# Performance work log

Measured on AMD Instinct MI355X. Metric: run time of the kernel, lower is better.

Reference implementation:

```python
import jax, jax.numpy as jnp
import numpy as np

B, N, IN, LAT, HID = 64, 128, 5, 3, 64
ALPHA = 0.1
NEG_SLOPE = 0.2  # GATv2Conv default negative_slope


def _w(key, fan_in, shape):
    return jax.random.normal(key, shape, jnp.float32) * (1.0 / np.sqrt(fan_in))


def setup_inputs():
    key = jax.random.key(0)
    ks = iter(jax.random.split(key, 64))
    d = {}
    d["batch"] = jax.random.normal(next(ks), (B, N, IN), jnp.float32)
    d["enc_w1"] = _w(next(ks), IN, (IN, HID));   d["enc_b1"] = jnp.zeros((HID,), jnp.float32)
    d["enc_w2"] = _w(next(ks), HID, (HID, HID)); d["enc_b2"] = jnp.zeros((HID,), jnp.float32)
    d["enc_w3"] = _w(next(ks), HID, (HID, LAT)); d["enc_b3"] = jnp.zeros((LAT,), jnp.float32)
    for i, cin in zip((1, 2, 3, 4), (1, HID, HID, HID)):
        d[f"g{i}_wl"] = _w(next(ks), cin, (cin, HID)); d[f"g{i}_bl"] = jnp.zeros((HID,), jnp.float32)
        d[f"g{i}_wr"] = _w(next(ks), cin, (cin, HID)); d[f"g{i}_br"] = jnp.zeros((HID,), jnp.float32)
        d[f"g{i}_att"] = _w(next(ks), HID, (HID,));    d[f"g{i}_b"] = jnp.zeros((HID,), jnp.float32)
    d["lab_w"] = _w(next(ks), HID, (HID, 4)); d["lab_b"] = jnp.zeros((4,), jnp.float32)
    d["val_w"] = _w(next(ks), HID, (HID, 1)); d["val_b"] = jnp.zeros((1,), jnp.float32)
    d["skip_w"] = _w(next(ks), LAT, (LAT, HID)); d["skip_b"] = jnp.zeros((HID,), jnp.float32)
    return d


def _gabriel_adj(p):
    """Gabriel graph adjacency, p: [N, LAT] -> bool [N, N] (symmetric, no diag).
    Edge (i,j) survives iff no witness k with |p_k - mid_ij|^2 < |p_i - p_j|^2 / 4."""
    n = p.shape[0]
    mid = 0.5 * (p[:, None, :] + p[None, :, :])                      # [n,n,d]
    r2 = 0.25 * jnp.sum((p[:, None, :] - p[None, :, :]) ** 2, -1)    # [n,n]
    pk2 = jnp.sum(p * p, -1)                                         # [n]
    m2 = jnp.sum(mid * mid, -1)                                      # [n,n]
    # d2[k,i,j] = |p_k - mid_ij|^2 via expansion (avoids [n,n,n,d] tensor)
    d2 = pk2[:, None, None] - 2.0 * jnp.einsum('kd,ijd->kij', p, mid) + m2[None]
    idx = jnp.arange(n)
    not_ij = (idx[:, None, None] != idx[None, :, None]) & (idx[:, None, None] != idx[None, None, :])
    blocked = jnp.any((d2 < r2[None]) & not_ij, axis=0)              # [n,n]
    return (~blocked) & (idx[:, None] != idx[None, :])


def _gatv2(x, adj, wl, bl, wr, br, att, b):
    """Dense single-head GATv2 (PyG GATv2Conv semantics, self-loops already in adj).
    x: [B,N,Cin], adj: bool [B,N,N] (adj[b,i,j] => edge j->i)."""
    hl = x @ wl + bl   # source transform (lin_l)
    hr = x @ wr + br   # target transform (lin_r)
    e = jax.nn.leaky_relu(hr[:, :, None, :] + hl[:, None, :, :], NEG_SLOPE)  # [B,i,j,H]
    s = jnp.einsum('bijh,h->bij', e, att)
    s = jnp.where(adj, s, -1e30)
    a = jax.nn.softmax(s, axis=-1)                                   # softmax over neighbors j of i
    return jnp.einsum('bij,bjh->bih', a, hl) + b


def reference(batch, enc_w1, enc_b1, enc_w2, enc_b2, enc_w3, enc_b3,
              g1_wl, g1_bl, g1_wr, g1_br, g1_att, g1_b,
              g2_wl, g2_bl, g2_wr, g2_br, g2_att, g2_b,
              g3_wl, g3_bl, g3_wr, g3_br, g3_att, g3_b,
              g4_wl, g4_bl, g4_wr, g4_br, g4_att, g4_b,
              lab_w, lab_b, val_w, val_b, skip_w, skip_b):
    relu = jax.nn.relu
    h = relu(batch @ enc_w1 + enc_b1)
    h = relu(h @ enc_w2 + enc_b2)
    latent = h @ enc_w3 + enc_b3                                     # [B,N,3]

    adj = jax.vmap(_gabriel_adj)(jax.lax.stop_gradient(latent))      # bool [B,N,N]
    adj_sl = adj | jnp.eye(N, dtype=bool)                            # add_self_loops=True

    x0 = latent[..., 2:3]                                            # node feature = 3rd latent coord
    x1 = relu(_gatv2(x0, adj_sl, g1_wl, g1_bl, g1_wr, g1_br, g1_att, g1_b))
    x2 = relu(_gatv2(x1, adj_sl, g2_wl, g2_bl, g2_wr, g2_br, g2_att, g2_b))
    skip = latent @ skip_w + skip_b
    x3 = relu(_gatv2(x2, adj_sl, g3_wl, g3_bl, g3_wr, g3_br, g3_att, g3_b) + ALPHA * skip)
    logits = x3 @ lab_w + lab_b                                      # [B,N,4]
    x4 = relu(_gatv2(x2, adj_sl, g4_wl, g4_bl, g4_wr, g4_br, g4_att, g4_b) + ALPHA * skip)
    values = x4 @ val_w + val_b                                      # [B,N,1]

    # dense edge attributes: pairwise latent distances masked by the Gabriel adjacency
    d2p = jnp.sum((latent[:, :, None, :] - latent[:, None, :, :]) ** 2, -1)
    edge_dist = jnp.sqrt(jnp.where(adj, d2p, 1.0)) * adj

    return (batch[:, :, :4], batch[:, :, 4:5], logits, values, latent, adj, edge_dist)
```

## Files before the change

### kernel.cpp

```cpp
#include <hip/hip_runtime.h>

#define BB 64
#define NN 128
#define INF_ 5
#define LATD 3
#define HIDD 64

__global__ __launch_bounds__(256) void enc_kernel(
    const float* __restrict__ batch,
    const float* __restrict__ w1, const float* __restrict__ b1,
    const float* __restrict__ w2, const float* __restrict__ b2,
    const float* __restrict__ w3, const float* __restrict__ b3,
    double* __restrict__ aos,
    float* __restrict__ o0, float* __restrict__ o1, float* __restrict__ o4)
{
    const int b = blockIdx.x;
    const int n0 = blockIdx.y * 32;
    const int tid = threadIdx.x;
    const int w = tid >> 6, lane = tid & 63;

    __shared__ double xs[32][6];
    __shared__ double w1s[INF_][HIDD];
    __shared__ float  w2s[HIDD * HIDD];
    __shared__ double w3s[HIDD][LATD];
    __shared__ double b1s[HIDD], b2s[HIDD], b3s[LATD];

    for (int idx = tid; idx < 32 * INF_; idx += 256) {
        int n = idx / INF_, c = idx % INF_;
        float v = batch[((size_t)b * NN + n0 + n) * INF_ + c];
        xs[n][c] = (double)v;
        if (c < 4) o0[((size_t)b * NN + n0 + n) * 4 + c] = v;
        else       o1[(size_t)b * NN + n0 + n] = v;
    }
    for (int idx = tid; idx < INF_ * HIDD; idx += 256)
        w1s[idx / HIDD][idx % HIDD] = (double)w1[idx];
    for (int idx = tid; idx < HIDD * HIDD; idx += 256)
        w2s[idx] = w2[idx];
    for (int idx = tid; idx < HIDD * LATD; idx += 256)
        w3s[idx / LATD][idx % LATD] = (double)w3[idx];
    if (tid < HIDD) {
        b1s[tid] = (double)b1[tid];
        b2s[tid] = (double)b2[tid];
    }
    if (tid < LATD) b3s[tid] = (double)b3[tid];
    __syncthreads();

    for (int r = 0; r < 8; ++r) {
        const int nl = w * 8 + r;
        const int n = n0 + nl;
        double h1v = b1s[lane];
        for (int k = 0; k < INF_; ++k) h1v += xs[nl][k] * w1s[k][lane];
        h1v = fmax(h1v, 0.0);
        double h2v = b2s[lane];
        for (int k = 0; k < HIDD; ++k) {
            double h1k = __shfl(h1v, k, 64);
            h2v += h1k * (double)w2s[k * HIDD + lane];
        }
        h2v = fmax(h2v, 0.0);
        double l0 = h2v * w3s[lane][0];
        double l1 = h2v * w3s[lane][1];
        double l2 = h2v * w3s[lane][2];
        for (int o = 32; o >= 1; o >>= 1) {
            l0 += __shfl_xor(l0, o, 64);
            l1 += __shfl_xor(l1, o, 64);
            l2 += __shfl_xor(l2, o, 64);
        }
        l0 += b3s[0]; l1 += b3s[1]; l2 += b3s[2];
        if (lane == 0) {
            double* A = aos + ((size_t)b * NN + n) * 4;
            A[0] = l0; A[1] = l1; A[2] = l2;
            A[3] = l0 * l0 + l1 * l1 + l2 * l2;
        }
        if (lane < LATD) {
            double lv = (lane == 0) ? l0 : ((lane == 1) ? l1 : l2);
            o4[((size_t)b * NN + n) * LATD + lane] = (float)lv;
        }
    }
}

__global__ __launch_bounds__(256) void gabriel_kernel(
    const double* __restrict__ aos,
    float* __restrict__ o5, float* __restrict__ o6)
{
    const int b = blockIdx.y;
    const int w = threadIdx.x >> 6, lane = threadIdx.x & 63;
    const int v = blockIdx.x * 4 + w;

    __shared__ double4 Ps[NN];
    const double2* src = (const double2*)(aos + (size_t)b * NN * 4);
    double2* dst = (double2*)Ps;
    for (int idx = threadIdx.x; idx < NN * 2; idx += 256) dst[idx] = src[idx];
    __syncthreads();

    const double4 A  = Ps[lane];
    const double4 Bq = Ps[lane + 64];

    for (int half = 0; half < 2; ++half) {
        const int i = (half == 0) ? v : 126 - v;
        if (half == 1 && i == v) break;
        const int jstart = (half == 0) ? (v + 1) : (127 - v);
        const double4 pi = Ps[i];
        const double aix = A.x - pi.x,  aiy = A.y - pi.y,  aiz = A.z - pi.z;
        const double bix = Bq.x - pi.x, biy = Bq.y - pi.y, biz = Bq.z - pi.z;
        const bool mA = (lane != i), mB = (lane + 64 != i);
        for (int j = jstart; j < NN; ++j) {
            double4 pj = Ps[j];
            double ajx = A.x - pj.x,  ajy = A.y - pj.y,  ajz = A.z - pj.z;
            double bjx = Bq.x - pj.x, bjy = Bq.y - pj.y, bjz = Bq.z - pj.z;
            double dA = aix * ajx + aiy * ajy + aiz * ajz;
            double dB = bix * bjx + biy * bjy + biz * bjz;
            bool tA = (dA < 0.0) && mA && (lane != j);
            bool tB = (dB < 0.0) && mB && (lane + 64 != j);
            if (!__any(tA || tB)) {
                if (lane == 0) {
                    double dx = pi.x - pj.x, dy = pi.y - pj.y, dz = pi.z - pj.z;
                    float d = (float)sqrt(dx * dx + dy * dy + dz * dz);
                    size_t ij = ((size_t)b * NN + i) * NN + j;
                    size_t ji = ((size_t)b * NN + j) * NN + i;
                    o5[ij] = 1.0f; o5[ji] = 1.0f;
                    o6[ij] = d;    o6[ji] = d;
                }
            }
        }
    }
}

template <int CIN>
__global__ __launch_bounds__(256) void lin_kernel(
    const float* __restrict__ xin,
    const float* __restrict__ latf,
    const float* __restrict__ wl, const float* __restrict__ bl,
    const float* __restrict__ wr, const float* __restrict__ br,
    float* __restrict__ hl, float* __restrict__ hr)
{
    const int bx = blockIdx.x;
    const int b = bx >> 2, n0 = (bx & 3) << 5;
    const int tid = threadIdx.x, w = tid >> 6, lane = tid & 63;
    __shared__ float4 xs4[(CIN == 64) ? 32 * 16 : 8];
    float* xsh = (float*)xs4;

    if constexpr (CIN == 64) {
        const float4* src = (const float4*)(xin + ((size_t)b * NN + n0) * HIDD);
        for (int idx = tid; idx < 32 * 16; idx += 256) xs4[idx] = src[idx];
    } else {
        if (tid < 32) xsh[tid] = latf[((size_t)b * NN + n0 + tid) * LATD + 2];
    }
    __syncthreads();

    float wc[CIN];
    #pragma unroll
    for (int k = 0; k < CIN; ++k) wc[k] = wl[k * HIDD + lane];
    float bv = bl[lane];
    for (int m = 0; m < 8; ++m) {
        int nl = w * 8 + m;
        float acc = bv;
        if constexpr (CIN == 64) {
            #pragma unroll
            for (int t = 0; t < 16; ++t) {
                float4 q = xs4[nl * 16 + t];
                acc = fmaf(q.x, wc[4 * t + 0], acc);
                acc = fmaf(q.y, wc[4 * t + 1], acc);
                acc = fmaf(q.z, wc[4 * t + 2], acc);
                acc = fmaf(q.w, wc[4 * t + 3], acc);
            }
        } else acc = fmaf(xsh[nl], wc[0], acc);
        hl[((size_t)b * NN + n0 + nl) * HIDD + lane] = acc;
    }
    #pragma unroll
    for (int k = 0; k < CIN; ++k) wc[k] = wr[k * HIDD + lane];
    bv = br[lane];
    for (int m = 0; m < 8; ++m) {
        int nl = w * 8 + m;
        float acc = bv;
        if constexpr (CIN == 64) {
            #pragma unroll
            for (int t = 0; t < 16; ++t) {
                float4 q = xs4[nl * 16 + t];
                acc = fmaf(q.x, wc[4 * t + 0], acc);
                acc = fmaf(q.y, wc[4 * t + 1], acc);
                acc = fmaf(q.z, wc[4 * t + 2], acc);
                acc = fmaf(q.w, wc[4 * t + 3], acc);
            }
        } else acc = fmaf(xsh[nl], wc[0], acc);
        hr[((size_t)b * NN + n0 + nl) * HIDD + lane] = acc;
    }
}

template <int C>
__global__ __launch_bounds__(256, 2) void attn_kernel(
    const float* __restrict__ hl, const float* __restrict__ hr,
    const float* __restrict__ att, const float* __restrict__ bias,
    const float* __restrict__ adjf,
    const float* __restrict__ latf,
    const float* __restrict__ skw, const float* __restrict__ skb,
    float* __restrict__ xout,
    const float* __restrict__ head_w, const float* __restrict__ head_b,
    float* __restrict__ head_out)
{
    const int bx = blockIdx.x;
    const int b = bx >> 3, i0 = (bx & 7) << 4;
    const int tid = threadIdx.x, w = tid >> 6, lane = tid & 63;

    __shared__ __align__(16) float hls[NN * 68];
    __shared__ __align__(16) float hrs[16 * HIDD];
    __shared__ float4 as4[4][NN];
    __shared__ __align__(16) float atts[HIDD];
    __shared__ float bsv[HIDD];
    __shared__ float hws[(C > 0) ? HIDD * C : 1], hbs[(C > 0) ? C : 1];
    __shared__ float sws[LATD * HIDD], sbs[HIDD];
    __shared__ float latr[16 * LATD];

    {
        const float4* src = (const float4*)(hl + (size_t)b * NN * HIDD);
        for (int idx = tid; idx < NN * 16; idx += 256) {
            int j = idx >> 4, c = idx & 15;
            *(float4*)&hls[j * 68 + 4 * c] = src[idx];
        }
        const float4* srcr = (const float4*)(hr + ((size_t)b * NN + i0) * HIDD);
        for (int idx = tid; idx < 16 * 16; idx += 256)
            ((float4*)hrs)[idx] = srcr[idx];
    }
    if (tid < HIDD) { atts[tid] = att[tid]; bsv[tid] = bias[tid]; }
    if constexpr (C > 0) {
        for (int idx = tid; idx < HIDD * C; idx += 256) hws[idx] = head_w[idx];
        if (tid < C) hbs[tid] = head_b[tid];
    }
    if (skw != nullptr) {
        for (int idx = tid; idx < LATD * HIDD; idx += 256) sws[idx] = skw[idx];
        if (tid < HIDD) sbs[tid] = skb[tid];
        if (tid < 16 * LATD) latr[tid] = latf[((size_t)b * NN + i0) * LATD + tid];
    }
    __syncthreads();

    float h0[HIDD], h1[HIDD];
    #pragma unroll
    for (int t = 0; t < 16; ++t) {
        float4 q0 = *(const float4*)&hls[lane * 68 + 4 * t];
        float4 q1 = *(const float4*)&hls[(lane + 64) * 68 + 4 * t];
        h0[4 * t + 0] = q0.x; h0[4 * t + 1] = q0.y; h0[4 * t + 2] = q0.z; h0[4 * t + 3] = q0.w;
        h1[4 * t + 0] = q1.x; h1[4 * t + 1] = q1.y; h1[4 * t + 2] = q1.z; h1[4 * t + 3] = q1.w;
    }

    float a0[4], a1[4];
    #pragma unroll
    for (int r = 0; r < 4; ++r) {
        const int il = w * 4 + r, i = i0 + il;
        float acc0 = 0.f, acc1 = 0.f;
        #pragma unroll
        for (int t = 0; t < 16; ++t) {
            float4 rv = *(const float4*)&hrs[il * HIDD + 4 * t];
            float4 av = *(const float4*)&atts[4 * t];
            float e;
            e = rv.x + h0[4 * t + 0]; e = (e > 0.f) ? e : 0.2f * e; acc0 = fmaf(av.x, e, acc0);
            e = rv.y + h0[4 * t + 1]; e = (e > 0.f) ? e : 0.2f * e; acc0 = fmaf(av.y, e, acc0);
            e = rv.z + h0[4 * t + 2]; e = (e > 0.f) ? e : 0.2f * e; acc0 = fmaf(av.z, e, acc0);
            e = rv.w + h0[4 * t + 3]; e = (e > 0.f) ? e : 0.2f * e; acc0 = fmaf(av.w, e, acc0);
            e = rv.x + h1[4 * t + 0]; e = (e > 0.f) ? e : 0.2f * e; acc1 = fmaf(av.x, e, acc1);
            e = rv.y + h1[4 * t + 1]; e = (e > 0.f) ? e : 0.2f * e; acc1 = fmaf(av.y, e, acc1);
            e = rv.z + h1[4 * t + 2]; e = (e > 0.f) ? e : 0.2f * e; acc1 = fmaf(av.z, e, acc1);
            e = rv.w + h1[4 * t + 3]; e = (e > 0.f) ? e : 0.2f * e; acc1 = fmaf(av.w, e, acc1);
        }
        const float* arow = adjf + ((size_t)b * NN + i) * NN;
        bool ad0 = (arow[lane] != 0.f)      || (lane == i);
        bool ad1 = (arow[lane + 64] != 0.f) || (lane + 64 == i);
        float s0 = ad0 ? acc0 : -1e30f;
        float s1 = ad1 ? acc1 : -1e30f;
        float mxv = fmaxf(s0, s1);
        for (int o = 32; o >= 1; o >>= 1) mxv = fmaxf(mxv, __shfl_xor(mxv, o, 64));
        float e0 = __expf(s0 - mxv), e1 = __expf(s1 - mxv);
        float sm = e0 + e1;
        for (int o = 32; o >= 1; o >>= 1) sm += __shfl_xor(sm, o, 64);
        float inv = 1.f / sm;
        a0[r] = e0 * inv;
        a1[r] = e1 * inv;
    }
    as4[w][lane]      = make_float4(a0[0], a0[1], a0[2], a0[3]);
    as4[w][lane + 64] = make_float4(a1[0], a1[1], a1[2], a1[3]);

    float acc[4] = {0.f, 0.f, 0.f, 0.f};
    for (int j = 0; j < NN; ++j) {
        float4 av = as4[w][j];
        float hv = hls[j * 68 + lane];
        acc[0] = fmaf(av.x, hv, acc[0]);
        acc[1] = fmaf(av.y, hv, acc[1]);
        acc[2] = fmaf(av.z, hv, acc[2]);
        acc[3] = fmaf(av.w, hv, acc[3]);
    }

    #pragma unroll
    for (int r = 0; r < 4; ++r) {
        const int il = w * 4 + r, i = i0 + il;
        float out = acc[r] + bsv[lane];
        if (skw != nullptr) {
            const float* lr = latr + il * LATD;
            float sk = sbs[lane];
            sk = fmaf(lr[0], sws[lane], sk);
            sk = fmaf(lr[1], sws[64 + lane], sk);
            sk = fmaf(lr[2], sws[128 + lane], sk);
            out += 0.1f * sk;
        }
        out = fmaxf(out, 0.f);
        if constexpr (C == 0) {
            xout[((size_t)b * NN + i) * HIDD + lane] = out;
        } else {
            float hv[C > 0 ? C : 1];
            #pragma unroll
            for (int c = 0; c < C; ++c) {
                float vv = out * hws[lane * C + c];
                for (int o = 32; o >= 1; o >>= 1) vv += __shfl_xor(vv, o, 64);
                hv[c] = vv + hbs[c];
            }
            if (lane == 0)
                for (int c = 0; c < C; ++c)
                    head_out[((size_t)b * NN + i) * C + c] = hv[c];
        }
    }
}

extern "C" void kernel_launch(void* const* d_in, const int* in_sizes, int n_in,
                              void* d_out, int out_size, void* d_ws, size_t ws_size,
                              hipStream_t stream)
{
    const float* batch  = (const float*)d_in[0];
    const float* enc_w1 = (const float*)d_in[1];
    const float* enc_b1 = (const float*)d_in[2];
    const float* enc_w2 = (const float*)d_in[3];
    const float* enc_b2 = (const float*)d_in[4];
    const float* enc_w3 = (const float*)d_in[5];
    const float* enc_b3 = (const float*)d_in[6];
    const float* g_wl[4]  = {(const float*)d_in[7],  (const float*)d_in[13], (const float*)d_in[19], (const float*)d_in[25]};
    const float* g_bl[4]  = {(const float*)d_in[8],  (const float*)d_in[14], (const float*)d_in[20], (const float*)d_in[26]};
    const float* g_wr[4]  = {(const float*)d_in[9],  (const float*)d_in[15], (const float*)d_in[21], (const float*)d_in[27]};
    const float* g_br[4]  = {(const float*)d_in[10], (const float*)d_in[16], (const float*)d_in[22], (const float*)d_in[28]};
    const float* g_att[4] = {(const float*)d_in[11], (const float*)d_in[17], (const float*)d_in[23], (const float*)d_in[29]};
    const float* g_b[4]   = {(const float*)d_in[12], (const float*)d_in[18], (const float*)d_in[24], (const float*)d_in[30]};
    const float* lab_w = (const float*)d_in[31];
    const float* lab_b = (const float*)d_in[32];
    const float* val_w = (const float*)d_in[33];
    const float* val_b = (const float*)d_in[34];
    const float* skw   = (const float*)d_in[35];
    const float* skb   = (const float*)d_in[36];

    float* out = (float*)d_out;
    float* o0 = out;
    float* o1 = out + 32768;
    float* o2 = out + 40960;
    float* o3 = out + 73728;
    float* o4 = out + 81920;
    float* o5 = out + 106496;
    float* o6 = out + 1155072;

    char* p = (char*)d_ws;
    auto carve = [&](size_t bytes) { void* r = (void*)p; p += (bytes + 255) & ~(size_t)255; return r; };
    double* aos = (double*)carve((size_t)BB * NN * 4 * 8);
    float*  xA  = (float*) carve((size_t)BB * NN * HIDD * 4);
    float*  xB  = (float*) carve((size_t)BB * NN * HIDD * 4);
    float*  hlw = (float*) carve((size_t)BB * NN * HIDD * 4);
    float*  hrw = (float*) carve((size_t)BB * NN * HIDD * 4);

    enc_kernel<<<dim3(BB, 4), 256, 0, stream>>>(batch, enc_w1, enc_b1, enc_w2, enc_b2,
                                                enc_w3, enc_b3, aos, o0, o1, o4);
    hipMemsetAsync(o5, 0, (size_t)2 * 1048576 * 4, stream);
    gabriel_kernel<<<dim3(16, BB), 256, 0, stream>>>(aos, o5, o6);

    lin_kernel<1><<<BB * 4, 256, 0, stream>>>(nullptr, o4, g_wl[0], g_bl[0], g_wr[0], g_br[0], hlw, hrw);
    attn_kernel<0><<<BB * 8, 256, 0, stream>>>(hlw, hrw, g_att[0], g_b[0], o5, o4,
                                               nullptr, nullptr, xA, nullptr, nullptr, nullptr);
    lin_kernel<64><<<BB * 4, 256, 0, stream>>>(xA, o4, g_wl[1], g_bl[1], g_wr[1], g_br[1], hlw, hrw);
    attn_kernel<0><<<BB * 8, 256, 0, stream>>>(hlw, hrw, g_att[1], g_b[1], o5, o4,
                                               nullptr, nullptr, xB, nullptr, nullptr, nullptr);
    lin_kernel<64><<<BB * 4, 256, 0, stream>>>(xB, o4, g_wl[2], g_bl[2], g_wr[2], g_br[2], hlw, hrw);
    attn_kernel<4><<<BB * 8, 256, 0, stream>>>(hlw, hrw, g_att[2], g_b[2], o5, o4,
                                               skw, skb, nullptr, lab_w, lab_b, o2);
    lin_kernel<64><<<BB * 4, 256, 0, stream>>>(xB, o4, g_wl[3], g_bl[3], g_wr[3], g_br[3], hlw, hrw);
    attn_kernel<1><<<BB * 8, 256, 0, stream>>>(hlw, hrw, g_att[3], g_b[3], o5, o4,
                                               skw, skb, nullptr, val_w, val_b, o3);
}
```

Measured before the change: 311.5 us.

## Store GAT projections as bf16, merge layer 3/4 kernels, split gabriel work

The hl/hr projections are now stored as packed bf16 instead of fp32, which halves that intermediate traffic. The separate layer-3 and layer-4 lin and attention launches are merged into single two-slice grids. The adjacency memset is folded into the encoder kernel, and the gabriel grid is doubled so each wave handles every other j. In the attention kernel, shared-memory broadcasts of hr, att and the attention weights are replaced with readlane-based cross-lane reads. The bf16 rounding of the projections changes numerics and may hurt accuracy, and the extra launch-level parallelism depends on occupancy.

```diff
diff --git a/kernel.cpp b/kernel.cpp
--- a/kernel.cpp
+++ b/kernel.cpp
@@ -5,6 +5,18 @@
 #define INF_ 5
 #define LATD 3
 #define HIDD 64
+
+__device__ __forceinline__ float bflo(unsigned u) { return __uint_as_float(u << 16); }
+__device__ __forceinline__ float bfhi(unsigned u) { return __uint_as_float(u & 0xffff0000u); }
+__device__ __forceinline__ unsigned bfpack(float a, float b) {
+    unsigned ua = __float_as_uint(a), ub = __float_as_uint(b);
+    unsigned ra = (ua + 0x7fffu + ((ua >> 16) & 1u)) >> 16;
+    unsigned rb = (ub + 0x7fffu + ((ub >> 16) & 1u)) >> 16;
+    return ra | (rb << 16);
+}
+__device__ __forceinline__ float rlane(float v, int l) {
+    return __int_as_float(__builtin_amdgcn_readlane(__float_as_int(v), l));
+}
 
 __global__ __launch_bounds__(256) void enc_kernel(
     const float* __restrict__ batch,
@@ -12,12 +24,20 @@
     const float* __restrict__ w2, const float* __restrict__ b2,
     const float* __restrict__ w3, const float* __restrict__ b3,
     double* __restrict__ aos,
-    float* __restrict__ o0, float* __restrict__ o1, float* __restrict__ o4)
+    float* __restrict__ o0, float* __restrict__ o1, float* __restrict__ o4,
+    float* __restrict__ o5)
 {
     const int b = blockIdx.x;
     const int n0 = blockIdx.y * 32;
     const int tid = threadIdx.x;
     const int w = tid >> 6, lane = tid & 63;
+
+    {
+        const int blk = blockIdx.x * 4 + blockIdx.y;
+        float4* z = (float4*)o5 + (size_t)blk * 2048;
+        float4 zero = make_float4(0.f, 0.f, 0.f, 0.f);
+        for (int q = tid; q < 2048; q += 256) z[q] = zero;
+    }
 
     __shared__ double xs[32][6];
     __shared__ double w1s[INF_][HIDD];
@@ -84,7 +104,8 @@
 {
     const int b = blockIdx.y;
     const int w = threadIdx.x >> 6, lane = threadIdx.x & 63;
-    const int v = blockIdx.x * 4 + w;
+    const int u = blockIdx.x * 4 + w;
+    const int v = u >> 1, par = u & 1;
 
     __shared__ double4 Ps[NN];
     const double2* src = (const double2*)(aos + (size_t)b * NN * 4);
@@ -99,11 +120,12 @@
         const int i = (half == 0) ? v : 126 - v;
         if (half == 1 && i == v) break;
         const int jstart = (half == 0) ? (v + 1) : (127 - v);
+        const int j0 = jstart + ((jstart ^ par) & 1);
         const double4 pi = Ps[i];
         const double aix = A.x - pi.x,  aiy = A.y - pi.y,  aiz = A.z - pi.z;
         const double bix = Bq.x - pi.x, biy = Bq.y - pi.y, biz = Bq.z - pi.z;
         const bool mA = (lane != i), mB = (lane + 64 != i);
-        for (int j = jstart; j < NN; ++j) {
+        for (int j = j0; j < NN; j += 2) {
             double4 pj = Ps[j];
             double ajx = A.x - pj.x,  ajy = A.y - pj.y,  ajz = A.z - pj.z;
             double bjx = Bq.x - pj.x, bjy = Bq.y - pj.y, bjz = Bq.z - pj.z;
@@ -126,19 +148,14 @@
 }
 
 template <int CIN>
-__global__ __launch_bounds__(256) void lin_kernel(
-    const float* __restrict__ xin,
-    const float* __restrict__ latf,
+__device__ __forceinline__ void lin_body(
+    int b, int n0, const float* __restrict__ xin, const float* __restrict__ latf,
     const float* __restrict__ wl, const float* __restrict__ bl,
     const float* __restrict__ wr, const float* __restrict__ br,
-    float* __restrict__ hl, float* __restrict__ hr)
-{
-    const int bx = blockIdx.x;
-    const int b = bx >> 2, n0 = (bx & 3) << 5;
-    const int tid = threadIdx.x, w = tid >> 6, lane = tid & 63;
-    __shared__ float4 xs4[(CIN == 64) ? 32 * 16 : 8];
+    unsigned* __restrict__ hlp, unsigned* __restrict__ hrp,
+    float4* xs4, int tid)
+{
     float* xsh = (float*)xs4;
-
     if constexpr (CIN == 64) {
         const float4* src = (const float4*)(xin + ((size_t)b * NN + n0) * HIDD);
         for (int idx = tid; idx < 32 * 16; idx += 256) xs4[idx] = src[idx];
@@ -147,6 +164,7 @@
     }
     __syncthreads();
 
+    const int w = tid >> 6, lane = tid & 63;
     float wc[CIN];
     #pragma unroll
     for (int k = 0; k < CIN; ++k) wc[k] = wl[k * HIDD + lane];
@@ -164,7 +182,9 @@
                 acc = fmaf(q.w, wc[4 * t + 3], acc);
             }
         } else acc = fmaf(xsh[nl], wc[0], acc);
-        hl[((size_t)b * NN + n0 + nl) * HIDD + lane] = acc;
+        float partner = __shfl_xor(acc, 1, 64);
+        if ((lane & 1) == 0)
+            hlp[((size_t)b * NN + n0 + nl) * 32 + (lane >> 1)] = bfpack(acc, partner);
     }
     #pragma unroll
     for (int k = 0; k < CIN; ++k) wc[k] = wr[k * HIDD + lane];
@@ -182,53 +202,77 @@
                 acc = fmaf(q.w, wc[4 * t + 3], acc);
             }
         } else acc = fmaf(xsh[nl], wc[0], acc);
-        hr[((size_t)b * NN + n0 + nl) * HIDD + lane] = acc;
-    }
+        float partner = __shfl_xor(acc, 1, 64);
+        if ((lane & 1) == 0)
+            hrp[((size_t)b * NN + n0 + nl) * 32 + (lane >> 1)] = bfpack(acc, partner);
+    }
+}
+
+template <int CIN>
+__global__ __launch_bounds__(256) void lin_kernel(
+    const float* __restrict__ xin, const float* __restrict__ latf,
+    const float* __restrict__ wl, const float* __restrict__ bl,
+    const float* __restrict__ wr, const float* __restrict__ br,
+    unsigned* __restrict__ hlp, unsigned* __restrict__ hrp)
+{
+    __shared__ float4 xs4[(CIN == 64) ? 32 * 16 : 8];
+    lin_body<CIN>(blockIdx.x >> 2, (blockIdx.x & 3) << 5, xin, latf,
+                  wl, bl, wr, br, hlp, hrp, xs4, threadIdx.x);
+}
+
+__global__ __launch_bounds__(256) void lin34_kernel(
+    const float* __restrict__ xin,
+    const float* __restrict__ wl3, const float* __restrict__ bl3,
+    const float* __restrict__ wr3, const float* __restrict__ br3,
+    const float* __restrict__ wl4, const float* __restrict__ bl4,
+    const float* __restrict__ wr4, const float* __restrict__ br4,
+    unsigned* __restrict__ hl3p, unsigned* __restrict__ hr3p,
+    unsigned* __restrict__ hl4p, unsigned* __restrict__ hr4p)
+{
+    __shared__ float4 xs4[32 * 16];
+    const int b = blockIdx.x >> 2, n0 = (blockIdx.x & 3) << 5;
+    if (blockIdx.y == 0)
+        lin_body<64>(b, n0, xin, nullptr, wl3, bl3, wr3, br3, hl3p, hr3p, xs4, threadIdx.x);
+    else
+        lin_body<64>(b, n0, xin, nullptr, wl4, bl4, wr4, br4, hl4p, hr4p, xs4, threadIdx.x);
 }
 
 template <int C>
-__global__ __launch_bounds__(256, 2) void attn_kernel(
-    const float* __restrict__ hl, const float* __restrict__ hr,
+__device__ __forceinline__ void attn_body(
+    int b, int i0, float* hls, int tid,
+    const unsigned* __restrict__ hlp, const unsigned* __restrict__ hrp,
     const float* __restrict__ att, const float* __restrict__ bias,
-    const float* __restrict__ adjf,
-    const float* __restrict__ latf,
+    const float* __restrict__ adjf, const float* __restrict__ latf,
     const float* __restrict__ skw, const float* __restrict__ skb,
     float* __restrict__ xout,
     const float* __restrict__ head_w, const float* __restrict__ head_b,
     float* __restrict__ head_out)
 {
-    const int bx = blockIdx.x;
-    const int b = bx >> 3, i0 = (bx & 7) << 4;
-    const int tid = threadIdx.x, w = tid >> 6, lane = tid & 63;
-
-    __shared__ __align__(16) float hls[NN * 68];
-    __shared__ __align__(16) float hrs[16 * HIDD];
-    __shared__ float4 as4[4][NN];
-    __shared__ __align__(16) float atts[HIDD];
-    __shared__ float bsv[HIDD];
-    __shared__ float hws[(C > 0) ? HIDD * C : 1], hbs[(C > 0) ? C : 1];
-    __shared__ float sws[LATD * HIDD], sbs[HIDD];
-    __shared__ float latr[16 * LATD];
+    const int w = tid >> 6, lane = tid & 63;
 
     {
-        const float4* src = (const float4*)(hl + (size_t)b * NN * HIDD);
-        for (int idx = tid; idx < NN * 16; idx += 256) {
-            int j = idx >> 4, c = idx & 15;
-            *(float4*)&hls[j * 68 + 4 * c] = src[idx];
-        }
-        const float4* srcr = (const float4*)(hr + ((size_t)b * NN + i0) * HIDD);
-        for (int idx = tid; idx < 16 * 16; idx += 256)
-            ((float4*)hrs)[idx] = srcr[idx];
-    }
-    if (tid < HIDD) { atts[tid] = att[tid]; bsv[tid] = bias[tid]; }
-    if constexpr (C > 0) {
-        for (int idx = tid; idx < HIDD * C; idx += 256) hws[idx] = head_w[idx];
-        if (tid < C) hbs[tid] = head_b[tid];
-    }
+        const uint4* src = (const uint4*)(hlp + (size_t)b * NN * 32);
+        for (int idx = tid; idx < NN * 8; idx += 256) {
+            int j = idx >> 3, q = idx & 7;
+            uint4 u4 = src[idx];
+            *(float4*)&hls[j * 68 + 8 * q] =
+                make_float4(bflo(u4.x), bfhi(u4.x), bflo(u4.y), bfhi(u4.y));
+            *(float4*)&hls[j * 68 + 8 * q + 4] =
+                make_float4(bflo(u4.z), bfhi(u4.z), bflo(u4.w), bfhi(u4.w));
+        }
+    }
+    float attv = att[lane];
+    float bsv  = bias[lane];
+    float hrv[4];
+    #pragma unroll
+    for (int r = 0; r < 4; ++r) {
+        unsigned u = hrp[((size_t)b * NN + i0 + w * 4 + r) * 32 + (lane >> 1)];
+        hrv[r] = (lane & 1) ? bfhi(u) : bflo(u);
+    }
+    float sw0 = 0.f, sw1 = 0.f, sw2 = 0.f, sbv = 0.f;
     if (skw != nullptr) {
-        for (int idx = tid; idx < LATD * HIDD; idx += 256) sws[idx] = skw[idx];
-        if (tid < HIDD) sbs[tid] = skb[tid];
-        if (tid < 16 * LATD) latr[tid] = latf[((size_t)b * NN + i0) * LATD + tid];
+        sw0 = skw[lane]; sw1 = skw[64 + lane]; sw2 = skw[128 + lane];
+        sbv = skb[lane];
     }
     __syncthreads();
 
@@ -244,21 +288,16 @@
     float a0[4], a1[4];
     #pragma unroll
     for (int r = 0; r < 4; ++r) {
-        const int il = w * 4 + r, i = i0 + il;
+        const int i = i0 + w * 4 + r;
         float acc0 = 0.f, acc1 = 0.f;
         #pragma unroll
-        for (int t = 0; t < 16; ++t) {
-            float4 rv = *(const float4*)&hrs[il * HIDD + 4 * t];
-            float4 av = *(const float4*)&atts[4 * t];
-            float e;
-            e = rv.x + h0[4 * t + 0]; e = (e > 0.f) ? e : 0.2f * e; acc0 = fmaf(av.x, e, acc0);
-            e = rv.y + h0[4 * t + 1]; e = (e > 0.f) ? e : 0.2f * e; acc0 = fmaf(av.y, e, acc0);
-            e = rv.z + h0[4 * t + 2]; e = (e > 0.f) ? e : 0.2f * e; acc0 = fmaf(av.z, e, acc0);
-            e = rv.w + h0[4 * t + 3]; e = (e > 0.f) ? e : 0.2f * e; acc0 = fmaf(av.w, e, acc0);
-            e = rv.x + h1[4 * t + 0]; e = (e > 0.f) ? e : 0.2f * e; acc1 = fmaf(av.x, e, acc1);
-            e = rv.y + h1[4 * t + 1]; e = (e > 0.f) ? e : 0.2f * e; acc1 = fmaf(av.y, e, acc1);
-            e = rv.z + h1[4 * t + 2]; e = (e > 0.f) ? e : 0.2f * e; acc1 = fmaf(av.z, e, acc1);
-            e = rv.w + h1[4 * t + 3]; e = (e > 0.f) ? e : 0.2f * e; acc1 = fmaf(av.w, e, acc1);
+        for (int h = 0; h < HIDD; ++h) {
+            float sh = rlane(hrv[r], h);
+            float av = rlane(attv, h);
+            float e0 = sh + h0[h]; e0 = (e0 > 0.f) ? e0 : 0.2f * e0;
+            float e1 = sh + h1[h]; e1 = (e1 > 0.f) ? e1 : 0.2f * e1;
+            acc0 = fmaf(av, e0, acc0);
+            acc1 = fmaf(av, e1, acc1);
         }
         const float* arow = adjf + ((size_t)b * NN + i) * NN;
         bool ad0 = (arow[lane] != 0.f)      || (lane == i);
@@ -274,29 +313,32 @@
         a0[r] = e0 * inv;
         a1[r] = e1 * inv;
     }
-    as4[w][lane]      = make_float4(a0[0], a0[1], a0[2], a0[3]);
-    as4[w][lane + 64] = make_float4(a1[0], a1[1], a1[2], a1[3]);
 
     float acc[4] = {0.f, 0.f, 0.f, 0.f};
-    for (int j = 0; j < NN; ++j) {
-        float4 av = as4[w][j];
+    #pragma unroll
+    for (int j = 0; j < 64; ++j) {
         float hv = hls[j * 68 + lane];
-        acc[0] = fmaf(av.x, hv, acc[0]);
-        acc[1] = fmaf(av.y, hv, acc[1]);
-        acc[2] = fmaf(av.z, hv, acc[2]);
-        acc[3] = fmaf(av.w, hv, acc[3]);
+        #pragma unroll
+        for (int r = 0; r < 4; ++r) acc[r] = fmaf(rlane(a0[r], j), hv, acc[r]);
+    }
+    #pragma unroll
+    for (int j = 0; j < 64; ++j) {
+        float hv = hls[(j + 64) * 68 + lane];
+        #pragma unroll
+        for (int r = 0; r < 4; ++r) acc[r] = fmaf(rlane(a1[r], j), hv, acc[r]);
     }
 
     #pragma unroll
     for (int r = 0; r < 4; ++r) {
         const int il = w * 4 + r, i = i0 + il;
-        float out = acc[r] + bsv[lane];
+        float out = acc[r] + bsv;
         if (skw != nullptr) {
-            const float* lr = latr + il * LATD;
-            float sk = sbs[lane];
-            sk = fmaf(lr[0], sws[lane], sk);
-            sk = fmaf(lr[1], sws[64 + lane], sk);
-            sk = fmaf(lr[2], sws[128 + lane], sk);
+            const float* lr = latf + ((size_t)b * NN + i) * LATD;
+            float l0v = lr[0], l1v = lr[1], l2v = lr[2];
+            float sk = sbv;
+            sk = fmaf(l0v, sw0, sk);
+            sk = fmaf(l1v, sw1, sk);
+            sk = fmaf(l2v, sw2, sk);
             out += 0.1f * sk;
         }
         out = fmaxf(out, 0.f);
@@ -306,15 +348,46 @@
             float hv[C > 0 ? C : 1];
             #pragma unroll
             for (int c = 0; c < C; ++c) {
-                float vv = out * hws[lane * C + c];
+                float vv = out * head_w[lane * C + c];
                 for (int o = 32; o >= 1; o >>= 1) vv += __shfl_xor(vv, o, 64);
-                hv[c] = vv + hbs[c];
+                hv[c] = vv + head_b[c];
             }
             if (lane == 0)
                 for (int c = 0; c < C; ++c)
                     head_out[((size_t)b * NN + i) * C + c] = hv[c];
         }
     }
+}
+
+__global__ __launch_bounds__(256, 2) void attn12_kernel(
+    const unsigned* __restrict__ hlp, const unsigned* __restrict__ hrp,
+    const float* __restrict__ att, const float* __restrict__ bias,
+    const float* __restrict__ adjf, float* __restrict__ xout)
+{
+    __shared__ __align__(16) float hls[NN * 68];
+    attn_body<0>(blockIdx.x >> 3, (blockIdx.x & 7) << 4, hls, threadIdx.x,
+                 hlp, hrp, att, bias, adjf, nullptr, nullptr, nullptr,
+                 xout, nullptr, nullptr, nullptr);
+}
+
+__global__ __launch_bounds__(256, 2) void attn34_kernel(
+    const unsigned* __restrict__ hl3p, const unsigned* __restrict__ hr3p,
+    const unsigned* __restrict__ hl4p, const unsigned* __restrict__ hr4p,
+    const float* __restrict__ att3, const float* __restrict__ b3,
+    const float* __restrict__ att4, const float* __restrict__ b4,
+    const float* __restrict__ adjf, const float* __restrict__ latf,
+    const float* __restrict__ skw, const float* __restrict__ skb,
+    const float* __restrict__ lab_w, const float* __restrict__ lab_b, float* __restrict__ o2,
+    const float* __restrict__ val_w, const float* __restrict__ val_b, float* __restrict__ o3)
+{
+    __shared__ __align__(16) float hls[NN * 68];
+    const int b = blockIdx.x >> 3, i0 = (blockIdx.x & 7) << 4;
+    if (blockIdx.y == 0)
+        attn_body<4>(b, i0, hls, threadIdx.x, hl3p, hr3p, att3, b3, adjf, latf,
+                     skw, skb, nullptr, lab_w, lab_b, o2);
+    else
+        attn_body<1>(b, i0, hls, threadIdx.x, hl4p, hr4p, att4, b4, adjf, latf,
+                     skw, skb, nullptr, val_w, val_b, o3);
 }
 
 extern "C" void kernel_launch(void* const* d_in, const int* in_sizes, int n_in,
@@ -352,27 +425,26 @@
 
     char* p = (char*)d_ws;
     auto carve = [&](size_t bytes) { void* r = (void*)p; p += (bytes + 255) & ~(size_t)255; return r; };
-    double* aos = (double*)carve((size_t)BB * NN * 4 * 8);
-    float*  xA  = (float*) carve((size_t)BB * NN * HIDD * 4);
-    float*  xB  = (float*) carve((size_t)BB * NN * HIDD * 4);
-    float*  hlw = (float*) carve((size_t)BB * NN * HIDD * 4);
-    float*  hrw = (float*) carve((size_t)BB * NN * HIDD * 4);
+    double*   aos  = (double*)  carve((size_t)BB * NN * 4 * 8);
+    float*    xA   = (float*)   carve((size_t)BB * NN * HIDD * 4);
+    float*    xB   = (float*)   carve((size_t)BB * NN * HIDD * 4);
+    unsigned* hlp  = (unsigned*)carve((size_t)BB * NN * 32 * 4);
+    unsigned* hrp  = (unsigned*)carve((size_t)BB * NN * 32 * 4);
+    unsigned* hl3p = (unsigned*)carve((size_t)BB * NN * 32 * 4);
+    unsigned* hr3p = (unsigned*)carve((size_t)BB * NN * 32 * 4);
 
     enc_kernel<<<dim3(BB, 4), 256, 0, stream>>>(batch, enc_w1, enc_b1, enc_w2, enc_b2,
-                                                enc_w3, enc_b3, aos, o0, o1, o4);
-    hipMemsetAsync(o5, 0, (size_t)2 * 1048576 * 4, stream);
-    gabriel_kernel<<<dim3(16, BB), 256, 0, stream>>>(aos, o5, o6);
-
-    lin_kernel<1><<<BB * 4, 256, 0, stream>>>(nullptr, o4, g_wl[0], g_bl[0], g_wr[0], g_br[0], hlw, hrw);
-    attn_kernel<0><<<BB * 8, 256, 0, stream>>>(hlw, hrw, g_att[0], g_b[0], o5, o4,
-                                               nullptr, nullptr, xA, nullptr, nullptr, nullptr);
-    lin_kernel<64><<<BB * 4, 256, 0, stream>>>(xA, o4, g_wl[1], g_bl[1], g_wr[1], g_br[1], hlw, hrw);
-    attn_kernel<0><<<BB * 8, 256, 0, stream>>>(hlw, hrw, g_att[1], g_b[1], o5, o4,
-                                               nullptr, nullptr, xB, nullptr, nullptr, nullptr);
-    lin_kernel<64><<<BB * 4, 256, 0, stream>>>(xB, o4, g_wl[2], g_bl[2], g_wr[2], g_br[2], hlw, hrw);
-    attn_kernel<4><<<BB * 8, 256, 0, stream>>>(hlw, hrw, g_att[2], g_b[2], o5, o4,
-                                               skw, skb, nullptr, lab_w, lab_b, o2);
-    lin_kernel<64><<<BB * 4, 256, 0, stream>>>(xB, o4, g_wl[3], g_bl[3], g_wr[3], g_br[3], hlw, hrw);
-    attn_kernel<1><<<BB * 8, 256, 0, stream>>>(hlw, hrw, g_att[3], g_b[3], o5, o4,
-                                               skw, skb, nullptr, val_w, val_b, o3);
-}
+                                                enc_w3, enc_b3, aos, o0, o1, o4, o5);
+    gabriel_kernel<<<dim3(32, BB), 256, 0, stream>>>(aos, o5, o6);
+
+    lin_kernel<1><<<BB * 4, 256, 0, stream>>>(nullptr, o4, g_wl[0], g_bl[0], g_wr[0], g_br[0], hlp, hrp);
+    attn12_kernel<<<BB * 8, 256, 0, stream>>>(hlp, hrp, g_att[0], g_b[0], o5, xA);
+    lin_kernel<64><<<BB * 4, 256, 0, stream>>>(xA, nullptr, g_wl[1], g_bl[1], g_wr[1], g_br[1], hlp, hrp);
+    attn12_kernel<<<BB * 8, 256, 0, stream>>>(hlp, hrp, g_att[1], g_b[1], o5, xB);
+    lin34_kernel<<<dim3(BB * 4, 2), 256, 0, stream>>>(xB,
+        g_wl[2], g_bl[2], g_wr[2], g_br[2], g_wl[3], g_bl[3], g_wr[3], g_br[3],
+        hl3p, hr3p, hlp, hrp);
+    attn34_kernel<<<dim3(BB * 8, 2), 256, 0, stream>>>(hl3p, hr3p, hlp, hrp,
+        g_att[2], g_b[2], g_att[3], g_b[3], o5, o4, skw, skb,
+        lab_w, lab_b, o2, val_w, val_b, o3);
+}
```

Measured after the change: 333.0 us. 6.9% more time.
